# Kernel optimization log

Measured on AMD Instinct MI355X. Metric: run time of the kernel, lower is better.

Reference implementation:

```python
import math
import jax, jax.numpy as jnp
import numpy as np

B, D, C = 1024, 512, 100000
S = 30.0
M = 0.3
COS_M = math.cos(M)
SIN_M = math.sin(M)
TH = math.cos(math.pi - M)
MM = math.sin(math.pi - M) * M
EPS = 1e-12  # torch F.normalize eps


def _l2norm(x):
    n = jnp.sqrt(jnp.sum(x * x, axis=-1, keepdims=True))
    return x / jnp.maximum(n, EPS)


def setup_inputs() -> dict:
    key = jax.random.key(0)
    k1, k2, k3 = jax.random.split(key, 3)
    features = jax.random.normal(k1, (B, D), dtype=jnp.float32)
    # xavier_uniform_ for weight [C, D]
    limit = math.sqrt(6.0 / (C + D))
    weight = jax.random.uniform(k2, (C, D), dtype=jnp.float32, minval=-limit, maxval=limit)
    targets = jax.random.randint(k3, (B,), 0, C, dtype=jnp.int64)
    return {"features": features, "weight": weight, "targets": targets}


def reference(features, weight, targets):
    # cosine similarity via normalized GEMM: [B, C]
    cosine = _l2norm(features) @ _l2norm(weight).T
    cosine = cosine.astype(jnp.float32)
    sine = jnp.sqrt(jnp.maximum(1.0 - cosine * cosine, 0.0))
    phi = cosine * COS_M - sine * SIN_M
    # easy_margin=False branch
    phi = jnp.where(cosine > TH, phi, cosine - MM)
    # one-hot blend (ls_eps == 0): target column gets phi, rest keep cosine
    one_hot = targets[:, None] == jnp.arange(C)[None, :]
    logits = jnp.where(one_hot, phi, cosine) * S
    # CrossEntropyLoss (mean reduction)
    logp = jax.nn.log_softmax(logits, axis=-1)
    loss = -jnp.mean(jnp.take_along_axis(logp, targets[:, None], axis=1))
    return loss
```

## Files before the change

### kernel.cpp

```cpp
#include <hip/hip_runtime.h>

#define B_ROWS 1024
#define D_DIM  512
#define C_CLS  100000
#define N_TILES 782
#define GRID_NJ 98

typedef unsigned short u16;
typedef __attribute__((ext_vector_type(8))) short bf16x8;
typedef __attribute__((ext_vector_type(4))) float f32x4;

__device__ __forceinline__ u16 f2bf(float f) {
  unsigned u = __float_as_uint(f);
  u += 0x7fffu + ((u >> 16) & 1u);
  return (u16)(u >> 16);
}

__device__ __forceinline__ bf16x8 pack8(float4 a, float4 b) {
  union { bf16x8 v; unsigned u[4]; } r;
  r.u[0] = __builtin_amdgcn_perm(__float_as_uint(a.y), __float_as_uint(a.x), 0x07060302u);
  r.u[1] = __builtin_amdgcn_perm(__float_as_uint(a.w), __float_as_uint(a.z), 0x07060302u);
  r.u[2] = __builtin_amdgcn_perm(__float_as_uint(b.y), __float_as_uint(b.x), 0x07060302u);
  r.u[3] = __builtin_amdgcn_perm(__float_as_uint(b.w), __float_as_uint(b.z), 0x07060302u);
  return r.v;
}

__device__ __forceinline__ void gll16(const void* g, void* l) {
  __builtin_amdgcn_global_load_lds(
      (const __attribute__((address_space(1))) unsigned int*)g,
      (__attribute__((address_space(3))) unsigned int*)l, 16, 0, 0);
}

__global__ __launch_bounds__(256) void prep_kernel(
    const float* __restrict__ feat, const float* __restrict__ wt,
    u16* __restrict__ fn, u16* __restrict__ wb, float* __restrict__ psum)
{
  const int lane  = threadIdx.x & 63;
  const int wid   = blockIdx.x * 4 + (threadIdx.x >> 6);
  const int nw    = gridDim.x * 4;
  const int total = B_ROWS + C_CLS;
  for (int row = wid; row < total; row += 2 * nw) {
    const int rowb  = row + nw;
    const bool hasb = rowb < total;
    const float* sa = (row < B_ROWS) ? feat + (size_t)row * D_DIM
                                     : wt + (size_t)(row - B_ROWS) * D_DIM;
    u16* da = (row < B_ROWS) ? fn + (size_t)row * D_DIM
                             : wb + (size_t)(row - B_ROWS) * D_DIM;
    const float* sb = sa;
    u16* db = da;
    if (hasb) {
      sb = (rowb < B_ROWS) ? feat + (size_t)rowb * D_DIM
                           : wt + (size_t)(rowb - B_ROWS) * D_DIM;
      db = (rowb < B_ROWS) ? fn + (size_t)rowb * D_DIM
                           : wb + (size_t)(rowb - B_ROWS) * D_DIM;
    }
    const float4 a0 = ((const float4*)sa)[2 * lane];
    const float4 a1 = ((const float4*)sa)[2 * lane + 1];
    const float4 b0 = ((const float4*)sb)[2 * lane];
    const float4 b1 = ((const float4*)sb)[2 * lane + 1];
    float ssa = a0.x*a0.x + a0.y*a0.y + a0.z*a0.z + a0.w*a0.w
              + a1.x*a1.x + a1.y*a1.y + a1.z*a1.z + a1.w*a1.w;
    float ssb = b0.x*b0.x + b0.y*b0.y + b0.z*b0.z + b0.w*b0.w
              + b1.x*b1.x + b1.y*b1.y + b1.z*b1.z + b1.w*b1.w;
#pragma unroll
    for (int m = 1; m < 64; m <<= 1) {
      ssa += __shfl_xor(ssa, m);
      ssb += __shfl_xor(ssb, m);
    }
    const float inva = 1.0f / fmaxf(sqrtf(ssa), 1e-12f);
    const float invb = 1.0f / fmaxf(sqrtf(ssb), 1e-12f);
    union { bf16x8 v; u16 e[8]; } oa, ob;
    oa.e[0] = f2bf(a0.x * inva); oa.e[1] = f2bf(a0.y * inva);
    oa.e[2] = f2bf(a0.z * inva); oa.e[3] = f2bf(a0.w * inva);
    oa.e[4] = f2bf(a1.x * inva); oa.e[5] = f2bf(a1.y * inva);
    oa.e[6] = f2bf(a1.z * inva); oa.e[7] = f2bf(a1.w * inva);
    ((bf16x8*)da)[lane] = oa.v;
    if (hasb) {
      ob.e[0] = f2bf(b0.x * invb); ob.e[1] = f2bf(b0.y * invb);
      ob.e[2] = f2bf(b0.z * invb); ob.e[3] = f2bf(b0.w * invb);
      ob.e[4] = f2bf(b1.x * invb); ob.e[5] = f2bf(b1.y * invb);
      ob.e[6] = f2bf(b1.z * invb); ob.e[7] = f2bf(b1.w * invb);
      ((bf16x8*)db)[lane] = ob.v;
    }
    if (row < B_ROWS && lane == 0) psum[row] = 0.0f;
  }
}

__global__ __launch_bounds__(256, 4) void arc_gemm_pre(
    const u16* __restrict__ fn, const u16* __restrict__ wb,
    const int* __restrict__ targets, float* __restrict__ psum,
    float* __restrict__ tlogit)
{
  __shared__ u16 As[2][128 * 32];
  __shared__ u16 Ws[2][128 * 32];
  __shared__ int tg[128];
  __shared__ float pr[256];

  const int tid = threadIdx.x;
  const int bx  = blockIdx.x;
  const int xcd = bx & 7;
  const int l   = bx >> 3;
  const int tile_ni = (l >> 3) * 8 + xcd;
  if (tile_ni >= N_TILES) return;
  const int tile_m = (l & 7) << 7;
  const int tile_n = tile_ni << 7;

  if (tid < 128) tg[tid] = targets[tile_m + tid];

  const int wave = tid >> 6, lane = tid & 63;
  const int wm = wave >> 1, wno = wave & 1;
  const int quad = lane >> 4, l15 = lane & 15;

  f32x4 acc[4][4] = {};

  const int srow   = tid >> 2;
  const int schunk = (tid & 3) ^ ((tid >> 3) & 3);
  const u16* Ag  = fn + (size_t)(tile_m + srow) * D_DIM + schunk * 8;
  const u16* Ag2 = Ag + 64 * D_DIM;
  const int wr0 = tile_n + srow;
  const int wr1 = wr0 + 64;
  const u16* Wg0 = wb + (size_t)min(wr0, C_CLS - 1) * D_DIM + schunk * 8;
  const u16* Wg1 = wb + (size_t)min(wr1, C_CLS - 1) * D_DIM + schunk * 8;

  const int rsw = (quad ^ ((l15 >> 1) & 3)) * 8;
  const u16* ApA = &As[0][(wm * 64 + l15) * 32 + rsw];
  const u16* ApW = &Ws[0][(wno * 64 + l15) * 32 + rsw];

  auto stage = [&](int b, int k0) {
    gll16(Ag  + k0, &As[b][tid * 8]);
    gll16(Ag2 + k0, &As[b][2048 + tid * 8]);
    gll16(Wg0 + k0, &Ws[b][tid * 8]);
    gll16(Wg1 + k0, &Ws[b][2048 + tid * 8]);
  };
  auto compute = [&](int b) {
    const u16* pA = ApA + b * 4096;
    const u16* pW = ApW + b * 4096;
    bf16x8 af[4], wf[4];
#pragma unroll
    for (int r = 0; r < 4; r++) af[r] = *(const bf16x8*)(pA + r * 512);
#pragma unroll
    for (int r = 0; r < 4; r++) wf[r] = *(const bf16x8*)(pW + r * 512);
#pragma unroll
    for (int rm = 0; rm < 4; rm++)
#pragma unroll
      for (int rn = 0; rn < 4; rn++)
        acc[rm][rn] = __builtin_amdgcn_mfma_f32_16x16x32_bf16(
            af[rm], wf[rn], acc[rm][rn], 0, 0, 0);
  };

  stage(0, 0);
  stage(1, 32);
  int cur = 0;
  for (int t = 0; t < 14; t++) {
    asm volatile("s_waitcnt vmcnt(4)" : : : "memory");
    __builtin_amdgcn_s_barrier();
    asm volatile("" : : : "memory");
    compute(cur);
    __builtin_amdgcn_s_barrier();
    asm volatile("" : : : "memory");
    stage(cur, (t + 2) * 32);
    cur ^= 1;
  }
  asm volatile("s_waitcnt vmcnt(4)" : : : "memory");
  __builtin_amdgcn_s_barrier();
  asm volatile("" : : : "memory");
  compute(cur);
  asm volatile("s_waitcnt vmcnt(0)" : : : "memory");
  __builtin_amdgcn_s_barrier();
  asm volatile("" : : : "memory");
  compute(cur ^ 1);

  const float Sc   = 30.0f;
  const float COSM = 0.9553364891256060f;
  const float SINM = 0.2955202066613396f;
  const float THc  = -0.9553364891256060f;
  const float MMc  = 0.0886560619984019f;

#pragma unroll
  for (int rm = 0; rm < 4; rm++) {
#pragma unroll
    for (int reg = 0; reg < 4; reg++) {
      const int bl = wm * 64 + rm * 16 + quad * 4 + reg;
      const int b = tile_m + bl;
      const int tgt = tg[bl];
      float s = 0.0f;
#pragma unroll
      for (int rn = 0; rn < 4; rn++) {
        const int c = tile_n + wno * 64 + rn * 16 + l15;
        const float cosv = acc[rm][rn][reg];
        float logit = Sc * cosv;
        if (c == tgt) {
          const float sine = sqrtf(fmaxf(1.0f - cosv * cosv, 0.0f));
          float phi = cosv * COSM - sine * SINM;
          phi = (cosv > THc) ? phi : (cosv - MMc);
          logit = Sc * phi;
          tlogit[b] = logit;
        }
        s += (c < C_CLS) ? __expf(logit - 30.0f) : 0.0f;
      }
      s += __shfl_xor(s, 1);
      s += __shfl_xor(s, 2);
      s += __shfl_xor(s, 4);
      s += __shfl_xor(s, 8);
      if (l15 == 0) pr[wno * 128 + bl] = s;
    }
  }
  __syncthreads();
  if (tid < 128) atomicAdd(psum + tile_m + tid, pr[tid] + pr[128 + tid]);
}

__global__ void norm_feat_kernel(const float* __restrict__ in,
                                 u16* __restrict__ out,
                                 float* __restrict__ psum)
{
  const int row  = blockIdx.x * 4 + (threadIdx.x >> 6);
  const int lane = threadIdx.x & 63;
  const float4* r = (const float4*)(in + (size_t)row * D_DIM);
  float4 v0 = r[lane];
  float4 v1 = r[lane + 64];
  float ss = v0.x*v0.x + v0.y*v0.y + v0.z*v0.z + v0.w*v0.w
           + v1.x*v1.x + v1.y*v1.y + v1.z*v1.z + v1.w*v1.w;
#pragma unroll
  for (int m = 1; m < 64; m <<= 1) ss += __shfl_xor(ss, m);
  const float inv = 1.0f / fmaxf(sqrtf(ss), 1e-12f);
  ushort4 o0, o1;
  o0.x = f2bf(v0.x * inv); o0.y = f2bf(v0.y * inv);
  o0.z = f2bf(v0.z * inv); o0.w = f2bf(v0.w * inv);
  o1.x = f2bf(v1.x * inv); o1.y = f2bf(v1.y * inv);
  o1.z = f2bf(v1.z * inv); o1.w = f2bf(v1.w * inv);
  ushort4* orow = (ushort4*)(out + (size_t)row * D_DIM);
  orow[lane]      = o0;
  orow[lane + 64] = o1;
  if (lane == 0) psum[row] = 0.0f;
}

__global__ __launch_bounds__(256, 4) void arc_gemm_raw(
    const u16* __restrict__ fn, const float* __restrict__ wt,
    const int* __restrict__ targets, float* __restrict__ psum,
    float* __restrict__ tlogit)
{
  __shared__ u16 As[128 * 32];
  __shared__ u16 Ws[128 * 32];
  __shared__ int tg[128];
  __shared__ float winv[128];

  const int tid = threadIdx.x;
  const int bx  = blockIdx.x;
  const int xcd = bx & 7;
  const int l   = bx >> 3;
  const int tile_ni = (l >> 3) * 8 + xcd;
  if (tile_ni >= N_TILES) return;
  const int tile_m = (l & 7) << 7;
  const int tile_n = tile_ni << 7;

  if (tid < 128) tg[tid] = targets[tile_m + tid];

  const int wave = tid >> 6, lane = tid & 63;
  const int wm = wave >> 1, wno = wave & 1;
  const int quad = lane >> 4, l15 = lane & 15;

  f32x4 acc[4][4] = {};

  const int srow   = tid >> 2;
  const int schunk = (tid & 3) ^ ((tid >> 3) & 3);
  const u16* Ag = fn + (size_t)(tile_m + srow) * D_DIM + schunk * 8;
  u16* Asd0 = As + tid * 8;
  u16* Asd1 = As + 2048 + tid * 8;
  const int wr0 = tile_n + srow;
  const int wr1 = wr0 + 64;
  const float* Wg0 = wt + (size_t)min(wr0, C_CLS - 1) * D_DIM + schunk * 8;
  const float* Wg1 = wt + (size_t)min(wr1, C_CLS - 1) * D_DIM + schunk * 8;
  u16* Wsd0 = Ws + tid * 8;
  u16* Wsd1 = Ws + 2048 + tid * 8;

  const int rsw = (quad ^ ((l15 >> 1) & 3)) * 8;
  const u16* ApA = As + (wm * 64 + l15) * 32 + rsw;
  const u16* ApW = Ws + (wno * 64 + l15) * 32 + rsw;

  float ssq0 = 0.0f, ssq1 = 0.0f;

  for (int k0 = 0; k0 < D_DIM; k0 += 32) {
    const float4 wa = *(const float4*)(Wg0 + k0);
    const float4 wb2 = *(const float4*)(Wg0 + k0 + 4);
    const float4 wc = *(const float4*)(Wg1 + k0);
    const float4 wd = *(const float4*)(Wg1 + k0 + 4);
    gll16(Ag + k0, Asd0);
    gll16(Ag + 64 * D_DIM + k0, Asd1);
    ssq0 += wa.x*wa.x + wa.y*wa.y + wa.z*wa.z + wa.w*wa.w
          + wb2.x*wb2.x + wb2.y*wb2.y + wb2.z*wb2.z + wb2.w*wb2.w;
    ssq1 += wc.x*wc.x + wc.y*wc.y + wc.z*wc.z + wc.w*wc.w
          + wd.x*wd.x + wd.y*wd.y + wd.z*wd.z + wd.w*wd.w;
    *(bf16x8*)Wsd0 = pack8(wa, wb2);
    *(bf16x8*)Wsd1 = pack8(wc, wd);
    __syncthreads();
    bf16x8 af[4], wf[4];
#pragma unroll
    for (int r = 0; r < 4; r++) af[r] = *(const bf16x8*)(ApA + r * 16 * 32);
#pragma unroll
    for (int r = 0; r < 4; r++) wf[r] = *(const bf16x8*)(ApW + r * 16 * 32);
#pragma unroll
    for (int rm = 0; rm < 4; rm++)
#pragma unroll
      for (int rn = 0; rn < 4; rn++)
        acc[rm][rn] = __builtin_amdgcn_mfma_f32_16x16x32_bf16(
            af[rm], wf[rn], acc[rm][rn], 0, 0, 0);
    __syncthreads();
  }

  ssq0 += __shfl_xor(ssq0, 1); ssq0 += __shfl_xor(ssq0, 2);
  ssq1 += __shfl_xor(ssq1, 1); ssq1 += __shfl_xor(ssq1, 2);
  if ((tid & 3) == 0) {
    winv[srow]      = 1.0f / fmaxf(sqrtf(ssq0), 1e-12f);
    winv[srow + 64] = 1.0f / fmaxf(sqrtf(ssq1), 1e-12f);
  }
  __syncthreads();

  float wiv[4];
#pragma unroll
  for (int rn = 0; rn < 4; rn++) wiv[rn] = winv[wno * 64 + rn * 16 + l15];

  const float Sc   = 30.0f;
  const float COSM = 0.9553364891256060f;
  const float SINM = 0.2955202066613396f;
  const float THc  = -0.9553364891256060f;
  const float MMc  = 0.0886560619984019f;

#pragma unroll
  for (int rm = 0; rm < 4; rm++) {
#pragma unroll
    for (int reg = 0; reg < 4; reg++) {
      const int bl = wm * 64 + rm * 16 + quad * 4 + reg;
      const int b = tile_m + bl;
      const int tgt = tg[bl];
      float s = 0.0f;
#pragma unroll
      for (int rn = 0; rn < 4; rn++) {
        const int c = tile_n + wno * 64 + rn * 16 + l15;
        const float cosv = acc[rm][rn][reg] * wiv[rn];
        float logit = Sc * cosv;
        if (c == tgt) {
          const float sine = sqrtf(fmaxf(1.0f - cosv * cosv, 0.0f));
          float phi = cosv * COSM - sine * SINM;
          phi = (cosv > THc) ? phi : (cosv - MMc);
          logit = Sc * phi;
          tlogit[b] = logit;
        }
        s += (c < C_CLS) ? __expf(logit - 30.0f) : 0.0f;
      }
      s += __shfl_xor(s, 1);
      s += __shfl_xor(s, 2);
      s += __shfl_xor(s, 4);
      s += __shfl_xor(s, 8);
      if (l15 == 0) atomicAdd(psum + b, s);
    }
  }
}

__global__ void finalize_loss(const float* __restrict__ psum,
                              const float* __restrict__ tlogit,
                              float* __restrict__ out)
{
  const int tid = threadIdx.x;
  float s = 0.0f;
  for (int i = tid; i < B_ROWS; i += 256)
    s += 30.0f + logf(psum[i]) - tlogit[i];
#pragma unroll
  for (int m = 1; m < 64; m <<= 1) s += __shfl_xor(s, m);
  __shared__ float red[4];
  if ((tid & 63) == 0) red[tid >> 6] = s;
  __syncthreads();
  if (tid == 0) out[0] = (red[0] + red[1] + red[2] + red[3]) * (1.0f / B_ROWS);
}

extern "C" void kernel_launch(void* const* d_in, const int* in_sizes, int n_in,
                              void* d_out, int out_size, void* d_ws, size_t ws_size,
                              hipStream_t stream) {
  const float* feat = (const float*)d_in[0];
  const float* wt   = (const float*)d_in[1];
  const int*   tgt  = (const int*)d_in[2];
  float* out = (float*)d_out;
  char* ws = (char*)d_ws;

  const size_t fn_bytes = (size_t)B_ROWS * D_DIM * 2;
  const size_t wb_bytes = (size_t)C_CLS * D_DIM * 2;
  const size_t tail     = 2 * (size_t)B_ROWS * sizeof(float);

  if (ws_size >= fn_bytes + wb_bytes + tail) {
    u16* fn = (u16*)ws;
    u16* wb = (u16*)(ws + fn_bytes);
    float* psum = (float*)(ws + fn_bytes + wb_bytes);
    float* tlogit = psum + B_ROWS;
    prep_kernel<<<2048, 256, 0, stream>>>(feat, wt, fn, wb, psum);
    arc_gemm_pre<<<GRID_NJ * 8 * 8, 256, 0, stream>>>(fn, wb, tgt, psum, tlogit);
    finalize_loss<<<1, 256, 0, stream>>>(psum, tlogit, out);
  } else {
    u16* fn = (u16*)ws;
    float* psum = (float*)(ws + fn_bytes);
    float* tlogit = psum + B_ROWS;
    norm_feat_kernel<<<B_ROWS / 4, 256, 0, stream>>>(feat, fn, psum);
    arc_gemm_raw<<<GRID_NJ * 8 * 8, 256, 0, stream>>>(fn, wt, tgt, psum, tlogit);
    finalize_loss<<<1, 256, 0, stream>>>(psum, tlogit, out);
  }
}
```

Measured before the change: 431.7 us.

## Replace 128x128 GEMM tile with 256x256 8-wave tile and interleaved prefetch

Replaces the 128x128x32 bf16 GEMM block with a 256x256x64 tile run by 512 threads (8 waves, each computing 128x64). Loads are staged in half-tiles interleaved with MFMA quarters, with barriers and s_setprio to overlap global-to-LDS copies with compute. The grid remap spreads tiles across XCDs. The larger tile raises arithmetic intensity and cuts redundant loads of the weight matrix, at the cost of more LDS, more registers, fewer resident blocks and padding waste on the last N tile.

Result: slower. 478.5 us (+10.8%).

```diff
diff --git a/kernel.cpp b/kernel.cpp
--- a/kernel.cpp
+++ b/kernel.cpp
@@ -5,6 +5,8 @@
 #define C_CLS  100000
 #define N_TILES 782
 #define GRID_NJ 98
+#define NT256 391
+#define GRID_256 1564
 
 typedef unsigned short u16;
 typedef __attribute__((ext_vector_type(8))) short bf16x8;
@@ -86,89 +88,119 @@
   }
 }
 
-__global__ __launch_bounds__(256, 4) void arc_gemm_pre(
+__global__ __launch_bounds__(512, 2) void arc_gemm_256(
     const u16* __restrict__ fn, const u16* __restrict__ wb,
     const int* __restrict__ targets, float* __restrict__ psum,
     float* __restrict__ tlogit)
 {
-  __shared__ u16 As[2][128 * 32];
-  __shared__ u16 Ws[2][128 * 32];
-  __shared__ int tg[128];
-  __shared__ float pr[256];
+  __shared__ u16 As[2 * 2 * 128 * 64];
+  __shared__ u16 Ws[2 * 2 * 128 * 64];
+  __shared__ int tg[256];
 
   const int tid = threadIdx.x;
-  const int bx  = blockIdx.x;
-  const int xcd = bx & 7;
-  const int l   = bx >> 3;
-  const int tile_ni = (l >> 3) * 8 + xcd;
-  if (tile_ni >= N_TILES) return;
-  const int tile_m = (l & 7) << 7;
-  const int tile_n = tile_ni << 7;
-
-  if (tid < 128) tg[tid] = targets[tile_m + tid];
-
-  const int wave = tid >> 6, lane = tid & 63;
-  const int wm = wave >> 1, wno = wave & 1;
+  const int orig = blockIdx.x;
+  const int xcd  = orig & 7;
+  const int wgid = (xcd < 4 ? xcd * 196 : 784 + (xcd - 4) * 195) + (orig >> 3);
+  const int tile_m = (wgid & 3) << 8;
+  const int tile_n = (wgid >> 2) << 8;
+
+  if (tid < 256) tg[tid] = targets[tile_m + tid];
+
+  const int lane = tid & 63;
+  const int wid  = tid >> 6;
+  const int wm = wid >> 2;
+  const int wn = wid & 3;
   const int quad = lane >> 4, l15 = lane & 15;
 
-  f32x4 acc[4][4] = {};
-
-  const int srow   = tid >> 2;
-  const int schunk = (tid & 3) ^ ((tid >> 3) & 3);
-  const u16* Ag  = fn + (size_t)(tile_m + srow) * D_DIM + schunk * 8;
-  const u16* Ag2 = Ag + 64 * D_DIM;
-  const int wr0 = tile_n + srow;
-  const int wr1 = wr0 + 64;
-  const u16* Wg0 = wb + (size_t)min(wr0, C_CLS - 1) * D_DIM + schunk * 8;
-  const u16* Wg1 = wb + (size_t)min(wr1, C_CLS - 1) * D_DIM + schunk * 8;
-
-  const int rsw = (quad ^ ((l15 >> 1) & 3)) * 8;
-  const u16* ApA = &As[0][(wm * 64 + l15) * 32 + rsw];
-  const u16* ApW = &Ws[0][(wno * 64 + l15) * 32 + rsw];
-
-  auto stage = [&](int b, int k0) {
-    gll16(Ag  + k0, &As[b][tid * 8]);
-    gll16(Ag2 + k0, &As[b][2048 + tid * 8]);
-    gll16(Wg0 + k0, &Ws[b][tid * 8]);
-    gll16(Wg1 + k0, &Ws[b][2048 + tid * 8]);
+  const int rowoff = tid >> 3;
+  const int chunkX = (tid & 7) ^ (rowoff & 7);
+  const size_t aBase = (size_t)(tile_m + rowoff) * D_DIM + chunkX * 8;
+  const unsigned wo00 = (unsigned)min(tile_n +   0 +  0 + rowoff, C_CLS - 1) * D_DIM + chunkX * 8;
+  const unsigned wo01 = (unsigned)min(tile_n +   0 + 64 + rowoff, C_CLS - 1) * D_DIM + chunkX * 8;
+  const unsigned wo10 = (unsigned)min(tile_n + 128 +  0 + rowoff, C_CLS - 1) * D_DIM + chunkX * 8;
+  const unsigned wo11 = (unsigned)min(tile_n + 128 + 64 + rowoff, C_CLS - 1) * D_DIM + chunkX * 8;
+  const int ldst = tid * 8;
+
+  auto stA = [&](int buf, int h, int kt) {
+    gll16(fn + aBase + (size_t)(h * 128) * D_DIM + kt * 64,
+          As + buf * 16384 + h * 8192 + ldst);
+    gll16(fn + aBase + (size_t)(h * 128 + 64) * D_DIM + kt * 64,
+          As + buf * 16384 + h * 8192 + 4096 + ldst);
   };
-  auto compute = [&](int b) {
-    const u16* pA = ApA + b * 4096;
-    const u16* pW = ApW + b * 4096;
-    bf16x8 af[4], wf[4];
-#pragma unroll
-    for (int r = 0; r < 4; r++) af[r] = *(const bf16x8*)(pA + r * 512);
-#pragma unroll
-    for (int r = 0; r < 4; r++) wf[r] = *(const bf16x8*)(pW + r * 512);
-#pragma unroll
-    for (int rm = 0; rm < 4; rm++)
-#pragma unroll
-      for (int rn = 0; rn < 4; rn++)
-        acc[rm][rn] = __builtin_amdgcn_mfma_f32_16x16x32_bf16(
-            af[rm], wf[rn], acc[rm][rn], 0, 0, 0);
+  auto stW = [&](int buf, int h, int kt) {
+    gll16(wb + (h ? wo10 : wo00) + kt * 64,
+          Ws + buf * 16384 + h * 8192 + ldst);
+    gll16(wb + (h ? wo11 : wo01) + kt * 64,
+          Ws + buf * 16384 + h * 8192 + 4096 + ldst);
   };
 
-  stage(0, 0);
-  stage(1, 32);
-  int cur = 0;
-  for (int t = 0; t < 14; t++) {
-    asm volatile("s_waitcnt vmcnt(4)" : : : "memory");
-    __builtin_amdgcn_s_barrier();
-    asm volatile("" : : : "memory");
-    compute(cur);
-    __builtin_amdgcn_s_barrier();
-    asm volatile("" : : : "memory");
-    stage(cur, (t + 2) * 32);
-    cur ^= 1;
-  }
-  asm volatile("s_waitcnt vmcnt(4)" : : : "memory");
-  __builtin_amdgcn_s_barrier();
-  asm volatile("" : : : "memory");
-  compute(cur);
-  asm volatile("s_waitcnt vmcnt(0)" : : : "memory");
-  __builtin_amdgcn_s_barrier();
-  asm volatile("" : : : "memory");
-  compute(cur ^ 1);
+  const int sw0 = (quad ^ (l15 & 7)) * 8;
+  const int rdA = wm * 8192 + l15 * 64 + sw0;
+  const int rdW = (wn >> 1) * 8192 + (wn & 1) * 4096 + l15 * 64 + sw0;
+
+  f32x4 acc[8][4] = {};
+  bf16x8 af[4][2], wf[4][2];
+
+  auto mfmaQ = [&](int mh, int ks) {
+    __builtin_amdgcn_s_setprio(1);
+#pragma unroll
+    for (int m = 0; m < 4; m++)
+#pragma unroll
+      for (int n = 0; n < 4; n++)
+        acc[mh * 4 + m][n] = __builtin_amdgcn_mfma_f32_16x16x32_bf16(
+            af[m][ks], wf[n][ks], acc[mh * 4 + m][n], 0, 0, 0);
+    __builtin_amdgcn_s_setprio(0);
+  };
+
+#define PBAR() __builtin_amdgcn_s_barrier()
+#define LGKM0_FENCE() do { \
+    asm volatile("s_waitcnt lgkmcnt(0)" ::: "memory"); \
+    __builtin_amdgcn_sched_barrier(0); } while (0)
+
+  stA(0, 0, 0); stA(0, 1, 0); stW(0, 0, 0); stW(0, 1, 0);
+  stW(1, 0, 1); stW(1, 1, 1); stA(1, 0, 1);
+  asm volatile("s_waitcnt vmcnt(6)" ::: "memory");
+  PBAR();
+
+  for (int c = 0; c < 8; ++c) {
+    const int bo = (c & 1) * 16384;
+#pragma unroll
+    for (int m = 0; m < 4; m++) {
+      af[m][0] = *(const bf16x8*)(As + bo + rdA + m * 1024);
+      af[m][1] = *(const bf16x8*)(As + bo + (rdA ^ 32) + m * 1024);
+    }
+#pragma unroll
+    for (int n = 0; n < 4; n++)
+      wf[n][0] = *(const bf16x8*)(Ws + bo + rdW + n * 1024);
+    if (c < 7) stA((c + 1) & 1, 1, c + 1);
+    PBAR(); LGKM0_FENCE();
+    mfmaQ(0, 0);
+    PBAR();
+#pragma unroll
+    for (int n = 0; n < 4; n++)
+      wf[n][1] = *(const bf16x8*)(Ws + bo + (rdW ^ 32) + n * 1024);
+    PBAR(); LGKM0_FENCE();
+    mfmaQ(0, 1);
+    PBAR();
+#pragma unroll
+    for (int m = 0; m < 4; m++) {
+      af[m][0] = *(const bf16x8*)(As + bo + rdA + (m + 4) * 1024);
+      af[m][1] = *(const bf16x8*)(As + bo + (rdA ^ 32) + (m + 4) * 1024);
+    }
+    if (c < 6) { stW(c & 1, 0, c + 2); stW(c & 1, 1, c + 2); }
+    PBAR(); LGKM0_FENCE();
+    mfmaQ(1, 0);
+    PBAR();
+    if (c < 6) {
+      stA(c & 1, 0, c + 2);
+      asm volatile("s_waitcnt vmcnt(6)" ::: "memory");
+    } else if (c == 6) {
+      asm volatile("s_waitcnt vmcnt(0)" ::: "memory");
+    }
+    PBAR();
+    mfmaQ(1, 1);
+    PBAR();
+  }
 
   const float Sc   = 30.0f;
   const float COSM = 0.9553364891256060f;
@@ -176,37 +208,41 @@
   const float THc  = -0.9553364891256060f;
   const float MMc  = 0.0886560619984019f;
 
-#pragma unroll
-  for (int rm = 0; rm < 4; rm++) {
+  float* pr = (float*)As;
+
+#pragma unroll
+  for (int m = 0; m < 8; m++) {
 #pragma unroll
     for (int reg = 0; reg < 4; reg++) {
-      const int bl = wm * 64 + rm * 16 + quad * 4 + reg;
+      const int bl = wm * 128 + m * 16 + quad * 4 + reg;
       const int b = tile_m + bl;
       const int tgt = tg[bl];
       float s = 0.0f;
 #pragma unroll
-      for (int rn = 0; rn < 4; rn++) {
-        const int c = tile_n + wno * 64 + rn * 16 + l15;
-        const float cosv = acc[rm][rn][reg];
+      for (int n = 0; n < 4; n++) {
+        const int cc = tile_n + wn * 64 + n * 16 + l15;
+        const float cosv = acc[m][n][reg];
         float logit = Sc * cosv;
-        if (c == tgt) {
+        if (cc == tgt) {
           const float sine = sqrtf(fmaxf(1.0f - cosv * cosv, 0.0f));
           float phi = cosv * COSM - sine * SINM;
           phi = (cosv > THc) ? phi : (cosv - MMc);
           logit = Sc * phi;
           tlogit[b] = logit;
         }
-        s += (c < C_CLS) ? __expf(logit - 30.0f) : 0.0f;
+        s += (cc < C_CLS) ? __expf(logit - 30.0f) : 0.0f;
       }
       s += __shfl_xor(s, 1);
       s += __shfl_xor(s, 2);
       s += __shfl_xor(s, 4);
       s += __shfl_xor(s, 8);
-      if (l15 == 0) pr[wno * 128 + bl] = s;
+      if (l15 == 0) pr[wn * 256 + bl] = s;
     }
   }
   __syncthreads();
-  if (tid < 128) atomicAdd(psum + tile_m + tid, pr[tid] + pr[128 + tid]);
+  if (tid < 256)
+    atomicAdd(psum + tile_m + tid,
+              pr[tid] + pr[256 + tid] + pr[512 + tid] + pr[768 + tid]);
 }
 
 __global__ void norm_feat_kernel(const float* __restrict__ in,
@@ -391,7 +427,7 @@
     float* psum = (float*)(ws + fn_bytes + wb_bytes);
     float* tlogit = psum + B_ROWS;
     prep_kernel<<<2048, 256, 0, stream>>>(feat, wt, fn, wb, psum);
-    arc_gemm_pre<<<GRID_NJ * 8 * 8, 256, 0, stream>>>(fn, wb, tgt, psum, tlogit);
+    arc_gemm_256<<<GRID_256, 512, 0, stream>>>(fn, wb, tgt, psum, tlogit);
     finalize_loss<<<1, 256, 0, stream>>>(psum, tlogit, out);
   } else {
     u16* fn = (u16*)ws;
```
